# Performance work log

Measured on AMD Instinct MI355X. Metric: run time of the kernel, lower is better.

## Reference

```python
import jax, jax.numpy as jnp
import numpy as np

# Faithful vectorization of the original Python-loop NDCG loss:
#  - score is normalized; predict_score is divided by sum of the (already
#    normalized) score, i.e. by ~1.0 (kept for exactness).
#  - For the j-th positive element (1-indexed inclusive count k), the loop
#    computes (p/(k+1) - s/log2(k+1))**2  [since DCGI[k-1] = s / log2(k+1)].
#  - For the j-th non-positive element (inclusive count m), with P total
#    positives, the loop computes (p/(P+m+1))**2.
#  - torch.mean of the scalar accumulator == the plain sum.

def setup_inputs() -> dict:
    key = jax.random.key(0)
    k1, k2 = jax.random.split(key)
    N = 16777216
    predict_score = jax.random.normal(k1, (N,), dtype=jnp.float32)
    score = jax.random.randint(k2, (N,), 0, 2).astype(jnp.float32)
    return {"predict_score": predict_score, "score": score}


def reference(predict_score, score):
    s = score / jnp.sum(score)                 # normalized relevance
    p = predict_score / jnp.sum(s)             # divide by ~1.0 (faithful)
    pos = s > 0.0
    posf = pos.astype(s.dtype)
    k = jnp.cumsum(posf)                       # inclusive positive rank
    m = jnp.cumsum(1.0 - posf)                 # inclusive negative rank
    P = k[-1]                                  # total number of positives
    # safe denominators at masked-out positions (avoid log2(1)=0 div)
    k_safe = jnp.maximum(k, 1.0)
    pos_term = (p / (k_safe + 1.0) - s / jnp.log2(k_safe + 1.0)) ** 2
    neg_term = (p / (P + m + 1.0)) ** 2
    loss = jnp.sum(jnp.where(pos, pos_term, neg_term))
    return loss
```

## Files before the change

### kernel.cpp

```cpp
#include <hip/hip_runtime.h>

#define TPB 256
#define PER_THREAD 32
#define CHUNK (TPB * PER_THREAD)

__device__ __forceinline__ unsigned block_excl_scan(unsigned tsum, unsigned* wtot) {
    const int lane = threadIdx.x & 63;
    const int wid  = threadIdx.x >> 6;
    unsigned v = tsum;
#pragma unroll
    for (int off = 1; off < 64; off <<= 1) {
        unsigned u = __shfl_up(v, off, 64);
        if (lane >= off) v += u;
    }
    if (lane == 63) wtot[wid] = v;
    __syncthreads();
    unsigned woff = 0;
    for (int w = 0; w < wid; ++w) woff += wtot[w];
    return woff + v - tsum;
}

__global__ void k_count(const float* __restrict__ score,
                        unsigned* __restrict__ blockCount,
                        unsigned* __restrict__ mask, long n) {
    const long base  = (long)blockIdx.x * CHUNK;
    const int  tid   = threadIdx.x;
    const long tbase = base + (long)tid * PER_THREAD;
    unsigned m = 0;
    if (tbase + PER_THREAD <= n) {
        const float4* s4 = reinterpret_cast<const float4*>(score + tbase);
#pragma unroll
        for (int q = 0; q < PER_THREAD / 4; ++q) {
            float4 v = s4[q];
            m |= ((unsigned)(v.x > 0.f)) << (4 * q + 0);
            m |= ((unsigned)(v.y > 0.f)) << (4 * q + 1);
            m |= ((unsigned)(v.z > 0.f)) << (4 * q + 2);
            m |= ((unsigned)(v.w > 0.f)) << (4 * q + 3);
        }
    } else {
        for (int e = 0; e < PER_THREAD; ++e) {
            long gi = tbase + e;
            if (gi < n && score[gi] > 0.f) m |= (1u << e);
        }
    }
    if (mask) mask[(size_t)blockIdx.x * TPB + tid] = m;

    unsigned cnt = __popc(m);
#pragma unroll
    for (int off = 32; off > 0; off >>= 1) cnt += __shfl_down(cnt, off, 64);
    __shared__ unsigned wsum[TPB / 64];
    const int lane = tid & 63, wid = tid >> 6;
    if (lane == 0) wsum[wid] = cnt;
    __syncthreads();
    if (tid == 0) {
        unsigned tot = 0;
        for (int w = 0; w < TPB / 64; ++w) tot += wsum[w];
        blockCount[blockIdx.x] = tot;
    }
}

template <bool USE_MASK>
__global__ void k_main(const float* __restrict__ predict,
                       const float* __restrict__ score,
                       const unsigned* __restrict__ mask,
                       const unsigned* __restrict__ blockCount,
                       double* __restrict__ blockSum, long n, int B) {
    const int  tid   = threadIdx.x;
    const int  bid   = blockIdx.x;
    const long base  = (long)bid * CHUNK;
    const long tbase = base + (long)tid * PER_THREAD;
    const int  lane  = tid & 63, wid = tid >> 6;

    __shared__ unsigned wtot[TPB / 64];
    __shared__ unsigned wpart[2 * (TPB / 64)];
    __shared__ unsigned s_off, s_P;
    __shared__ double   dsum[TPB / 64];

    const bool full = (tbase + PER_THREAD <= n);

    unsigned m = 0;
    if (USE_MASK) {
        m = mask[(size_t)bid * TPB + tid];
    } else {
        if (full) {
            const float4* s4 = reinterpret_cast<const float4*>(score + tbase);
#pragma unroll
            for (int q = 0; q < PER_THREAD / 4; ++q) {
                float4 v = s4[q];
                m |= ((unsigned)(v.x > 0.f)) << (4 * q + 0);
                m |= ((unsigned)(v.y > 0.f)) << (4 * q + 1);
                m |= ((unsigned)(v.z > 0.f)) << (4 * q + 2);
                m |= ((unsigned)(v.w > 0.f)) << (4 * q + 3);
            }
        } else {
            for (int e = 0; e < PER_THREAD; ++e) {
                long gi = tbase + e;
                if (gi < n && score[gi] > 0.f) m |= (1u << e);
            }
        }
    }

    unsigned cnt  = __popc(m);
    unsigned excl = block_excl_scan(cnt, wtot);

    unsigned offp = 0, tot = 0;
    for (int j = tid; j < B; j += TPB) {
        unsigned c = blockCount[j];
        tot  += c;
        offp += (j < bid) ? c : 0u;
    }
#pragma unroll
    for (int off = 32; off > 0; off >>= 1) {
        offp += __shfl_down(offp, off, 64);
        tot  += __shfl_down(tot,  off, 64);
    }
    if (lane == 0) { wpart[2 * wid] = offp; wpart[2 * wid + 1] = tot; }
    __syncthreads();
    if (tid == 0) {
        unsigned o = 0, t = 0;
        for (int w = 0; w < TPB / 64; ++w) { o += wpart[2 * w]; t += wpart[2 * w + 1]; }
        s_off = o; s_P = t;
    }
    __syncthreads();

    const unsigned P = s_P;
    const float invS = 1.0f / (float)P;
    const float sumS = (float)((double)invS * (double)P);
    const float rcpSumS = 1.0f / sumS;
    const float Pf = (float)P;
    unsigned run = s_off + excl;

    double acc = 0.0;
    if (full) {
        const float4* p4 = reinterpret_cast<const float4*>(predict + tbase);
#pragma unroll
        for (int q = 0; q < PER_THREAD / 4; ++q) {
            float4 pv4 = p4[q];
            float pv[4] = {pv4.x, pv4.y, pv4.z, pv4.w};
#pragma unroll
            for (int j = 0; j < 4; ++j) {
                const int e = 4 * q + j;
                const bool ispos = (m >> e) & 1u;
                const unsigned newrun = run + (ispos ? 1u : 0u);
                const float p = pv[j] * rcpSumS;
                const float kp1  = (float)(newrun + 1u);
                const float posv = p * __builtin_amdgcn_rcpf(kp1)
                                 - invS * __builtin_amdgcn_rcpf(__log2f(kp1));
                const unsigned mr = (unsigned)(tbase + e + 1) - newrun;
                const float negv  = p * __builtin_amdgcn_rcpf(Pf + (float)mr + 1.0f);
                const float t = ispos ? posv : negv;
                acc += (double)(t * t);
                run = newrun;
            }
        }
    } else {
        for (int e = 0; e < PER_THREAD; ++e) {
            long gi = tbase + e;
            if (gi >= n) break;
            const bool ispos = (m >> e) & 1u;
            const unsigned newrun = run + (ispos ? 1u : 0u);
            const float p = predict[gi] * rcpSumS;
            const float kp1  = (float)(newrun + 1u);
            const float posv = p * __builtin_amdgcn_rcpf(kp1)
                             - invS * __builtin_amdgcn_rcpf(__log2f(kp1));
            const unsigned mr = (unsigned)(gi + 1) - newrun;
            const float negv  = p * __builtin_amdgcn_rcpf(Pf + (float)mr + 1.0f);
            const float t = ispos ? posv : negv;
            acc += (double)(t * t);
            run = newrun;
        }
    }

#pragma unroll
    for (int off = 32; off > 0; off >>= 1) acc += __shfl_down(acc, off, 64);
    if (lane == 0) dsum[wid] = acc;
    __syncthreads();
    if (tid == 0) {
        double t = 0.0;
        for (int w = 0; w < TPB / 64; ++w) t += dsum[w];
        blockSum[bid] = t;
    }
}

__global__ void k_final(const double* __restrict__ blockSum,
                        float* __restrict__ out, int B) {
    const int tid = threadIdx.x;
    double acc = 0.0;
    for (int j = tid; j < B; j += TPB) acc += blockSum[j];
#pragma unroll
    for (int off = 32; off > 0; off >>= 1) acc += __shfl_down(acc, off, 64);
    __shared__ double dsum[TPB / 64];
    const int lane = tid & 63, wid = tid >> 6;
    if (lane == 0) dsum[wid] = acc;
    __syncthreads();
    if (tid == 0) {
        double tot = 0.0;
        for (int w = 0; w < TPB / 64; ++w) tot += dsum[w];
        out[0] = (float)tot;
    }
}

extern "C" void kernel_launch(void* const* d_in, const int* in_sizes, int n_in,
                              void* d_out, int out_size, void* d_ws, size_t ws_size,
                              hipStream_t stream) {
    const float* predict = (const float*)d_in[0];
    const float* score   = (const float*)d_in[1];
    const long n = (long)in_sizes[0];
    const int B = (int)((n + CHUNK - 1) / CHUNK);

    unsigned char* ws = (unsigned char*)d_ws;
    size_t off = 0;
    unsigned* blockCount = (unsigned*)(ws + off); off += (size_t)B * sizeof(unsigned);
    off = (off + 255) & ~(size_t)255;
    double*   blockSum   = (double*)(ws + off);   off += (size_t)B * sizeof(double);
    off = (off + 255) & ~(size_t)255;
    unsigned* maskBuf    = (unsigned*)(ws + off);
    const size_t maskBytes = (size_t)B * TPB * sizeof(unsigned);
    const bool useMask = (off + maskBytes) <= ws_size;

    k_count<<<B, TPB, 0, stream>>>(score, blockCount, useMask ? maskBuf : nullptr, n);
    if (useMask)
        k_main<true><<<B, TPB, 0, stream>>>(predict, nullptr, maskBuf, blockCount,
                                            blockSum, n, B);
    else
        k_main<false><<<B, TPB, 0, stream>>>(predict, score, nullptr, blockCount,
                                             blockSum, n, B);
    k_final<<<1, TPB, 0, stream>>>(blockSum, (float*)d_out, B);
}
```

Baseline: 41.92 us.

## Coalesce score/predict loads by wave-interleaved float4 access with shuffled mask nibbles

Result: faster. 35.51 us (-15.3%).

```diff
diff --git a/kernel.cpp b/kernel.cpp
--- a/kernel.cpp
+++ b/kernel.cpp
@@ -3,6 +3,8 @@
 #define TPB 256
 #define PER_THREAD 32
 #define CHUNK (TPB * PER_THREAD)
+#define WCHUNK (64 * PER_THREAD)
+#define NQ 8
 
 __device__ __forceinline__ unsigned block_excl_scan(unsigned tsum, unsigned* wtot) {
     const int lane = threadIdx.x & 63;
@@ -23,38 +25,53 @@
 __global__ void k_count(const float* __restrict__ score,
                         unsigned* __restrict__ blockCount,
                         unsigned* __restrict__ mask, long n) {
+    const int  tid  = threadIdx.x;
+    const int  lane = tid & 63, w = tid >> 6;
     const long base  = (long)blockIdx.x * CHUNK;
-    const int  tid   = threadIdx.x;
-    const long tbase = base + (long)tid * PER_THREAD;
-    unsigned m = 0;
-    if (tbase + PER_THREAD <= n) {
-        const float4* s4 = reinterpret_cast<const float4*>(score + tbase);
-#pragma unroll
-        for (int q = 0; q < PER_THREAD / 4; ++q) {
-            float4 v = s4[q];
-            m |= ((unsigned)(v.x > 0.f)) << (4 * q + 0);
-            m |= ((unsigned)(v.y > 0.f)) << (4 * q + 1);
-            m |= ((unsigned)(v.z > 0.f)) << (4 * q + 2);
-            m |= ((unsigned)(v.w > 0.f)) << (4 * q + 3);
+    const long wbase = base + (long)w * WCHUNK;
+    unsigned cnt = 0;
+
+    if (base + CHUNK <= n) {
+        const float4* s4 = reinterpret_cast<const float4*>(score);
+#pragma unroll
+        for (int q = 0; q < NQ; ++q) {
+            float4 v = s4[wbase / 4 + 64 * q + lane];
+            unsigned nib = (unsigned)(v.x > 0.f)        | ((unsigned)(v.y > 0.f) << 1)
+                         | ((unsigned)(v.z > 0.f) << 2) | ((unsigned)(v.w > 0.f) << 3);
+            cnt += __popc(nib);
+            unsigned part = nib << ((lane & 7) * 4);
+            part |= __shfl_xor(part, 1);
+            part |= __shfl_xor(part, 2);
+            part |= __shfl_xor(part, 4);
+            if ((lane & 7) == 0 && mask)
+                mask[(wbase >> 5) + 8 * q + (lane >> 3)] = part;
         }
     } else {
-        for (int e = 0; e < PER_THREAD; ++e) {
-            long gi = tbase + e;
-            if (gi < n && score[gi] > 0.f) m |= (1u << e);
-        }
-    }
-    if (mask) mask[(size_t)blockIdx.x * TPB + tid] = m;
-
-    unsigned cnt = __popc(m);
+        for (int q = 0; q < NQ; ++q) {
+            unsigned nib = 0;
+#pragma unroll
+            for (int j = 0; j < 4; ++j) {
+                long gi = wbase + 256 * q + 4 * lane + j;
+                if (gi < n && score[gi] > 0.f) nib |= (1u << j);
+            }
+            cnt += __popc(nib);
+            unsigned part = nib << ((lane & 7) * 4);
+            part |= __shfl_xor(part, 1);
+            part |= __shfl_xor(part, 2);
+            part |= __shfl_xor(part, 4);
+            if ((lane & 7) == 0 && mask)
+                mask[(wbase >> 5) + 8 * q + (lane >> 3)] = part;
+        }
+    }
+
 #pragma unroll
     for (int off = 32; off > 0; off >>= 1) cnt += __shfl_down(cnt, off, 64);
     __shared__ unsigned wsum[TPB / 64];
-    const int lane = tid & 63, wid = tid >> 6;
-    if (lane == 0) wsum[wid] = cnt;
+    if (lane == 0) wsum[w] = cnt;
     __syncthreads();
     if (tid == 0) {
         unsigned tot = 0;
-        for (int w = 0; w < TPB / 64; ++w) tot += wsum[w];
+        for (int i = 0; i < TPB / 64; ++i) tot += wsum[i];
         blockCount[blockIdx.x] = tot;
     }
 }
@@ -65,42 +82,42 @@
                        const unsigned* __restrict__ mask,
                        const unsigned* __restrict__ blockCount,
                        double* __restrict__ blockSum, long n, int B) {
-    const int  tid   = threadIdx.x;
-    const int  bid   = blockIdx.x;
+    const int  tid  = threadIdx.x;
+    const int  bid  = blockIdx.x;
+    const int  lane = tid & 63, w = tid >> 6;
     const long base  = (long)bid * CHUNK;
-    const long tbase = base + (long)tid * PER_THREAD;
-    const int  lane  = tid & 63, wid = tid >> 6;
+    const long wbase = base + (long)w * WCHUNK;
+    const bool full  = (base + CHUNK <= n);
 
     __shared__ unsigned wtot[TPB / 64];
     __shared__ unsigned wpart[2 * (TPB / 64)];
     __shared__ unsigned s_off, s_P;
     __shared__ double   dsum[TPB / 64];
 
-    const bool full = (tbase + PER_THREAD <= n);
-
-    unsigned m = 0;
+    unsigned wd = 0;
     if (USE_MASK) {
-        m = mask[(size_t)bid * TPB + tid];
+        wd = mask[(size_t)bid * TPB + tid];
     } else {
-        if (full) {
-            const float4* s4 = reinterpret_cast<const float4*>(score + tbase);
+        const long tb = base + (long)tid * PER_THREAD;
+        if (tb + PER_THREAD <= n) {
+            const float4* s4 = reinterpret_cast<const float4*>(score + tb);
 #pragma unroll
             for (int q = 0; q < PER_THREAD / 4; ++q) {
                 float4 v = s4[q];
-                m |= ((unsigned)(v.x > 0.f)) << (4 * q + 0);
-                m |= ((unsigned)(v.y > 0.f)) << (4 * q + 1);
-                m |= ((unsigned)(v.z > 0.f)) << (4 * q + 2);
-                m |= ((unsigned)(v.w > 0.f)) << (4 * q + 3);
+                wd |= ((unsigned)(v.x > 0.f)) << (4 * q + 0);
+                wd |= ((unsigned)(v.y > 0.f)) << (4 * q + 1);
+                wd |= ((unsigned)(v.z > 0.f)) << (4 * q + 2);
+                wd |= ((unsigned)(v.w > 0.f)) << (4 * q + 3);
             }
         } else {
             for (int e = 0; e < PER_THREAD; ++e) {
-                long gi = tbase + e;
-                if (gi < n && score[gi] > 0.f) m |= (1u << e);
-            }
-        }
-    }
-
-    unsigned cnt  = __popc(m);
+                long gi = tb + e;
+                if (gi < n && score[gi] > 0.f) wd |= (1u << e);
+            }
+        }
+    }
+
+    unsigned cnt  = __popc(wd);
     unsigned excl = block_excl_scan(cnt, wtot);
 
     unsigned offp = 0, tot = 0;
@@ -114,11 +131,11 @@
         offp += __shfl_down(offp, off, 64);
         tot  += __shfl_down(tot,  off, 64);
     }
-    if (lane == 0) { wpart[2 * wid] = offp; wpart[2 * wid + 1] = tot; }
+    if (lane == 0) { wpart[2 * w] = offp; wpart[2 * w + 1] = tot; }
     __syncthreads();
     if (tid == 0) {
         unsigned o = 0, t = 0;
-        for (int w = 0; w < TPB / 64; ++w) { o += wpart[2 * w]; t += wpart[2 * w + 1]; }
+        for (int i = 0; i < TPB / 64; ++i) { o += wpart[2 * i]; t += wpart[2 * i + 1]; }
         s_off = o; s_P = t;
     }
     __syncthreads();
@@ -128,56 +145,71 @@
     const float sumS = (float)((double)invS * (double)P);
     const float rcpSumS = 1.0f / sumS;
     const float Pf = (float)P;
-    unsigned run = s_off + excl;
+
+    const unsigned pre = s_off + excl;
 
     double acc = 0.0;
     if (full) {
-        const float4* p4 = reinterpret_cast<const float4*>(predict + tbase);
-#pragma unroll
-        for (int q = 0; q < PER_THREAD / 4; ++q) {
-            float4 pv4 = p4[q];
+        const float4* p4 = reinterpret_cast<const float4*>(predict);
+#pragma unroll
+        for (int q = 0; q < NQ; ++q) {
+            const int t = 8 * q + (lane >> 3);
+            const unsigned wq  = __shfl(wd,  t, 64);
+            const unsigned prq = __shfl(pre, t, 64);
+            const int nibStart = (lane & 7) * 4;
+            unsigned run = prq + __popc(wq & ((1u << nibStart) - 1u));
+            const unsigned nib = (wq >> nibStart) & 0xFu;
+            float4 pv4 = p4[wbase / 4 + 64 * q + lane];
             float pv[4] = {pv4.x, pv4.y, pv4.z, pv4.w};
 #pragma unroll
             for (int j = 0; j < 4; ++j) {
-                const int e = 4 * q + j;
-                const bool ispos = (m >> e) & 1u;
+                const bool ispos = (nib >> j) & 1u;
                 const unsigned newrun = run + (ispos ? 1u : 0u);
+                const long gi = wbase + 256 * q + 4 * lane + j;
                 const float p = pv[j] * rcpSumS;
                 const float kp1  = (float)(newrun + 1u);
                 const float posv = p * __builtin_amdgcn_rcpf(kp1)
                                  - invS * __builtin_amdgcn_rcpf(__log2f(kp1));
-                const unsigned mr = (unsigned)(tbase + e + 1) - newrun;
+                const unsigned mr = (unsigned)(gi + 1) - newrun;
                 const float negv  = p * __builtin_amdgcn_rcpf(Pf + (float)mr + 1.0f);
-                const float t = ispos ? posv : negv;
-                acc += (double)(t * t);
+                const float tt = ispos ? posv : negv;
+                acc += (double)(tt * tt);
                 run = newrun;
             }
         }
     } else {
-        for (int e = 0; e < PER_THREAD; ++e) {
-            long gi = tbase + e;
-            if (gi >= n) break;
-            const bool ispos = (m >> e) & 1u;
-            const unsigned newrun = run + (ispos ? 1u : 0u);
-            const float p = predict[gi] * rcpSumS;
-            const float kp1  = (float)(newrun + 1u);
-            const float posv = p * __builtin_amdgcn_rcpf(kp1)
-                             - invS * __builtin_amdgcn_rcpf(__log2f(kp1));
-            const unsigned mr = (unsigned)(gi + 1) - newrun;
-            const float negv  = p * __builtin_amdgcn_rcpf(Pf + (float)mr + 1.0f);
-            const float t = ispos ? posv : negv;
-            acc += (double)(t * t);
-            run = newrun;
+        for (int q = 0; q < NQ; ++q) {
+            const int t = 8 * q + (lane >> 3);
+            const unsigned wq  = __shfl(wd,  t, 64);
+            const unsigned prq = __shfl(pre, t, 64);
+            const int nibStart = (lane & 7) * 4;
+            unsigned run = prq + __popc(wq & ((1u << nibStart) - 1u));
+            const unsigned nib = (wq >> nibStart) & 0xFu;
+            for (int j = 0; j < 4; ++j) {
+                const long gi = wbase + 256 * q + 4 * lane + j;
+                if (gi >= n) continue;
+                const bool ispos = (nib >> j) & 1u;
+                const unsigned newrun = run + (ispos ? 1u : 0u);
+                const float p = predict[gi] * rcpSumS;
+                const float kp1  = (float)(newrun + 1u);
+                const float posv = p * __builtin_amdgcn_rcpf(kp1)
+                                 - invS * __builtin_amdgcn_rcpf(__log2f(kp1));
+                const unsigned mr = (unsigned)(gi + 1) - newrun;
+                const float negv  = p * __builtin_amdgcn_rcpf(Pf + (float)mr + 1.0f);
+                const float tt = ispos ? posv : negv;
+                acc += (double)(tt * tt);
+                run = newrun;
+            }
         }
     }
 
 #pragma unroll
     for (int off = 32; off > 0; off >>= 1) acc += __shfl_down(acc, off, 64);
-    if (lane == 0) dsum[wid] = acc;
+    if (lane == 0) dsum[w] = acc;
     __syncthreads();
     if (tid == 0) {
         double t = 0.0;
-        for (int w = 0; w < TPB / 64; ++w) t += dsum[w];
+        for (int i = 0; i < TPB / 64; ++i) t += dsum[i];
         blockSum[bid] = t;
     }
 }
```
